# Kernel tuning notes

Measured on AMD Instinct MI355X. Metric: run time of the kernel, lower is better.

The kernel has to match this reference:

```python
import jax, jax.numpy as jnp
import numpy as np

B, C, H, W = 4, 64, 64, 64

def setup_inputs() -> dict:
    key = jax.random.key(0)
    ks = jax.random.split(key, 7)
    s = 1.0 / np.sqrt(C)
    return {
        "x": jax.random.normal(ks[0], (B, C, H, W), dtype=jnp.float32),
        "Wq": jax.random.normal(ks[1], (C, C), dtype=jnp.float32) * s,
        "bq": jax.random.normal(ks[2], (C,), dtype=jnp.float32) * s,
        "Wk": jax.random.normal(ks[3], (C, C), dtype=jnp.float32) * s,
        "bk": jax.random.normal(ks[4], (C,), dtype=jnp.float32) * s,
        "Wv": jax.random.normal(ks[5], (C, C), dtype=jnp.float32) * s,
        "bv": jax.random.normal(ks[6], (C,), dtype=jnp.float32) * s,
    }

def reference(x, Wq, bq, Wk, bk, Wv, bv):
    b, c, h, w = x.shape
    n = h * w
    xf = x.reshape(b, c, n)                                   # (B,C,N)
    # 1x1 convs == per-pixel linear maps over channels
    q = jnp.einsum('oc,bcn->bon', Wq, xf) + bq[None, :, None]  # (B,C,N)
    k = jnp.einsum('oc,bcn->bon', Wk, xf) + bk[None, :, None]  # (B,C,N)
    v = jnp.einsum('oc,bcn->bon', Wv, xf) + bv[None, :, None]  # (B,C,N)
    # energy = Q^T K : (B,N,N); note: no 1/sqrt(C) scaling in the original
    energy = jnp.einsum('bcn,bcm->bnm', q, k)
    attention = jax.nn.softmax(energy, axis=-1)
    # out = V @ attention^T : out[:, :, i] = sum_j V[:, :, j] * attention[i, j]
    out = jnp.einsum('bcm,bnm->bcn', v, attention)
    return out.reshape(b, c, h, w)
```

## Files before the change

kernel.cpp:

```cpp
#include <hip/hip_runtime.h>
#include <math.h>

#define T_N 4096
#define T_C 64
#define T_B 4
#define NSLICE 4
#define TILES_PER_SLICE (64 / NSLICE)

typedef __attribute__((ext_vector_type(8))) _Float16 f16x8;
typedef __attribute__((ext_vector_type(4))) _Float16 f16x4;
typedef __attribute__((ext_vector_type(4))) float f32x4;

__device__ inline unsigned short f2h(float f) {
    union { _Float16 h; unsigned short s; } u; u.h = (_Float16)f; return u.s;
}
__device__ inline float h2f(unsigned short s) {
    union { unsigned short s; _Float16 h; } u; u.s = s; return (float)u.h;
}

__global__ __launch_bounds__(256) void qkv_kernel(
    const float* __restrict__ x,
    const float* __restrict__ Wq, const float* __restrict__ bq,
    const float* __restrict__ Wk, const float* __restrict__ bk,
    const float* __restrict__ Wv, const float* __restrict__ bv,
    unsigned short* __restrict__ qt_hi, unsigned short* __restrict__ qt_lo,
    unsigned short* __restrict__ kt, unsigned short* __restrict__ vb)
{
    __shared__ __align__(16) unsigned short xsh[64 * 72];
    __shared__ __align__(16) unsigned short xsl[64 * 72];
    __shared__ __align__(16) unsigned short wf[64 * 72];

    const int tid = threadIdx.x;
    const int n0  = blockIdx.x * 64;
    const int b   = blockIdx.y;
    const int p   = blockIdx.z;
    const float* W    = (p == 0) ? Wq : (p == 1) ? Wk : Wv;
    const float* bias = (p == 0) ? bq : (p == 1) ? bk : bv;
    const float* xb   = x + (size_t)b * T_C * T_N;

    for (int i = tid; i < 1024; i += 256) {
        const int o = i >> 4, c4 = (i & 15) * 4;
        const float4 w4 = ((const float4*)W)[i];
        f16x4 wh;
        wh[0] = (_Float16)w4.x; wh[1] = (_Float16)w4.y;
        wh[2] = (_Float16)w4.z; wh[3] = (_Float16)w4.w;
        *(f16x4*)&wf[o * 72 + c4] = wh;
    }
    for (int i = tid; i < 1024; i += 256) {
        const int c = i >> 4, nj4 = (i & 15) * 4;
        const float4 xv = *(const float4*)&xb[c * T_N + n0 + nj4];
        const float xa[4] = {xv.x, xv.y, xv.z, xv.w};
        #pragma unroll
        for (int j = 0; j < 4; ++j) {
            const unsigned short h = f2h(xa[j]);
            xsh[(nj4 + j) * 72 + c] = h;
            xsl[(nj4 + j) * 72 + c] = f2h(xa[j] - h2f(h));
        }
    }
    __syncthreads();

    const int wv_  = tid >> 6;
    const int lane = tid & 63;
    const int quad = lane >> 4;
    const int col  = lane & 15;
    const size_t bN = (size_t)b * T_N;

    f16x8 xh[2], xl[2];
    #pragma unroll
    for (int s = 0; s < 2; ++s) {
        xh[s] = *(const f16x8*)&xsh[(wv_ * 16 + col) * 72 + s * 32 + quad * 8];
        xl[s] = *(const f16x8*)&xsl[(wv_ * 16 + col) * 72 + s * 32 + quad * 8];
    }

    #pragma unroll
    for (int osub = 0; osub < 4; ++osub) {
        f32x4 acc = (f32x4){0.f, 0.f, 0.f, 0.f};
        #pragma unroll
        for (int s = 0; s < 2; ++s) {
            const f16x8 wfr = *(const f16x8*)&wf[(osub * 16 + col) * 72 + s * 32 + quad * 8];
            acc = __builtin_amdgcn_mfma_f32_16x16x32_f16(xh[s], wfr, acc, 0, 0, 0);
            acc = __builtin_amdgcn_mfma_f32_16x16x32_f16(xl[s], wfr, acc, 0, 0, 0);
        }
        const float bb = bias[osub * 16 + col];
        if (p == 0) {
            #pragma unroll
            for (int r = 0; r < 4; ++r) {
                const float f = acc[r] + bb;
                const unsigned short h = f2h(f);
                const size_t off = (bN + n0 + wv_ * 16 + quad * 4 + r) * 64 + osub * 16 + col;
                qt_hi[off] = h;
                qt_lo[off] = f2h(f - h2f(h));
            }
        } else if (p == 1) {
            #pragma unroll
            for (int r = 0; r < 4; ++r)
                kt[(bN + n0 + wv_ * 16 + quad * 4 + r) * 64 + osub * 16 + col] =
                    f2h(acc[r] + bb);
        } else {
            union { ushort4 v; unsigned short s[4]; } hv;
            #pragma unroll
            for (int r = 0; r < 4; ++r) hv.s[r] = f2h(acc[r] + bb);
            *(ushort4*)&vb[((size_t)(b * 64 + osub * 16 + col)) * T_N +
                           n0 + wv_ * 16 + quad * 4] = hv.v;
        }
    }
}

__global__ __launch_bounds__(256, 4) void attn_kernel(
    const unsigned short* __restrict__ qt_hi, const unsigned short* __restrict__ qt_lo,
    const unsigned short* __restrict__ kt, const unsigned short* __restrict__ vb,
    unsigned short* __restrict__ o_part, float* __restrict__ mp, float* __restrict__ lp)
{
    __shared__ __align__(16) unsigned short ks[64 * 72];
    __shared__ __align__(16) unsigned short vs[64 * 72];

    const int tid   = threadIdx.x;
    const int n0    = blockIdx.x * 64;
    const int slice = blockIdx.y;
    const int b     = blockIdx.z;
    const int wv_   = tid >> 6;
    const int lane  = tid & 63;
    const int quad  = lane >> 4;
    const int col   = lane & 15;

    const size_t bN = (size_t)b * T_N;
    const int q_own = n0 + wv_ * 16 + col;

    f16x8 qh[2], ql[2];
    #pragma unroll
    for (int s = 0; s < 2; ++s) {
        const size_t qoff = (bN + q_own) * 64 + s * 32 + quad * 8;
        qh[s] = *(const f16x8*)&qt_hi[qoff];
        ql[s] = *(const f16x8*)&qt_lo[qoff];
    }

    f32x4 O[4];
    #pragma unroll
    for (int t = 0; t < 4; ++t) O[t] = (f32x4){0.f, 0.f, 0.f, 0.f};
    float m_st = -INFINITY, l_st = 0.f;

    for (int it = 0; it < TILES_PER_SLICE; ++it) {
        const int m0 = (slice * TILES_PER_SLICE + it) * 64;
        __syncthreads();
        for (int i = tid; i < 1024; i += 256) {
            if (i < 512) {
                const int row = i >> 3, cc = i & 7;
                *(float4*)&ks[row * 72 + cc * 8] =
                    *(const float4*)&kt[(bN + m0 + row) * 64 + cc * 8];
            } else {
                const int j = i - 512, row = j >> 3, cc = j & 7;
                *(float4*)&vs[row * 72 + cc * 8] =
                    *(const float4*)&vb[((size_t)(b * 64 + row)) * T_N + m0 + cc * 8];
            }
        }
        __syncthreads();

        f32x4 acc[4];
        #pragma unroll
        for (int t = 0; t < 4; ++t) acc[t] = (f32x4){0.f, 0.f, 0.f, 0.f};
        #pragma unroll
        for (int s = 0; s < 2; ++s) {
            #pragma unroll
            for (int t = 0; t < 4; ++t) {
                const f16x8 kf =
                    *(const f16x8*)&ks[(t * 16 + col) * 72 + s * 32 + quad * 8];
                acc[t] = __builtin_amdgcn_mfma_f32_16x16x32_f16(kf, qh[s], acc[t], 0, 0, 0);
                acc[t] = __builtin_amdgcn_mfma_f32_16x16x32_f16(kf, ql[s], acc[t], 0, 0, 0);
            }
        }

        float mx = -INFINITY;
        #pragma unroll
        for (int t = 0; t < 4; ++t)
            #pragma unroll
            for (int r = 0; r < 4; ++r) mx = fmaxf(mx, acc[t][r]);
        mx = fmaxf(mx, __shfl_xor(mx, 16));
        mx = fmaxf(mx, __shfl_xor(mx, 32));
        const float mnew = fmaxf(m_st, mx);
        const float alpha = __expf(m_st - mnew);
        float sum = 0.f;
        f16x4 pf[4];
        #pragma unroll
        for (int t = 0; t < 4; ++t) {
            #pragma unroll
            for (int r = 0; r < 4; ++r) {
                const float pv = __expf(acc[t][r] - mnew);
                sum += pv;
                pf[t][r] = (_Float16)pv;
            }
        }
        sum += __shfl_xor(sum, 16);
        sum += __shfl_xor(sum, 32);
        l_st = alpha * l_st + sum;
        m_st = mnew;

        #pragma unroll
        for (int tc = 0; tc < 4; ++tc) {
            O[tc] *= alpha;
            #pragma unroll
            for (int t = 0; t < 4; ++t) {
                const f16x4 vf =
                    *(const f16x4*)&vs[(tc * 16 + col) * 72 + t * 16 + quad * 4];
                O[tc] = __builtin_amdgcn_mfma_f32_16x16x16f16(vf, pf[t], O[tc], 0, 0, 0);
            }
        }
    }

    #pragma unroll
    for (int tc = 0; tc < 4; ++tc) {
        #pragma unroll
        for (int r = 0; r < 4; ++r) {
            o_part[((size_t)((slice * T_B + b) * 64 + tc * 16 + quad * 4 + r)) * T_N +
                   q_own] = f2h(O[tc][r]);
        }
    }
    if (quad == 0) {
        const size_t off = (size_t)(slice * T_B + b) * T_N + q_own;
        mp[off] = m_st;
        lp[off] = l_st;
    }
}

__global__ __launch_bounds__(256) void combine_kernel(
    const unsigned short* __restrict__ o_part,
    const float* __restrict__ mp, const float* __restrict__ lp,
    float* __restrict__ out)
{
    __shared__ float wn[NSLICE][32];

    const int tid = threadIdx.x;
    const int n0  = blockIdx.x * 32;
    const int b   = blockIdx.y;

    if (tid < 32) {
        float m_s[NSLICE], l_s[NSLICE];
        #pragma unroll
        for (int s = 0; s < NSLICE; ++s) {
            const size_t off = (size_t)(s * T_B + b) * T_N + n0 + tid;
            m_s[s] = mp[off];
            l_s[s] = lp[off];
        }
        float M = m_s[0];
        #pragma unroll
        for (int s = 1; s < NSLICE; ++s) M = fmaxf(M, m_s[s]);
        float w_s[NSLICE], L = 0.f;
        #pragma unroll
        for (int s = 0; s < NSLICE; ++s) {
            w_s[s] = __expf(m_s[s] - M);
            L += l_s[s] * w_s[s];
        }
        const float inv = 1.f / L;
        #pragma unroll
        for (int s = 0; s < NSLICE; ++s) wn[s][tid] = w_s[s] * inv;
    }
    __syncthreads();

    for (int t = tid; t < 512; t += 256) {
        const int c = t >> 3, g = t & 7;
        float4 acc = make_float4(0.f, 0.f, 0.f, 0.f);
        #pragma unroll
        for (int s = 0; s < NSLICE; ++s) {
            const ushort4 o4 = *(const ushort4*)
                &o_part[((size_t)((s * T_B + b) * 64 + c)) * T_N + n0 + g * 4];
            acc.x = fmaf(h2f(o4.x), wn[s][g * 4 + 0], acc.x);
            acc.y = fmaf(h2f(o4.y), wn[s][g * 4 + 1], acc.y);
            acc.z = fmaf(h2f(o4.z), wn[s][g * 4 + 2], acc.z);
            acc.w = fmaf(h2f(o4.w), wn[s][g * 4 + 3], acc.w);
        }
        *(float4*)&out[((size_t)(b * 64 + c)) * T_N + n0 + g * 4] = acc;
    }
}

extern "C" void kernel_launch(void* const* d_in, const int* in_sizes, int n_in,
                              void* d_out, int out_size, void* d_ws, size_t ws_size,
                              hipStream_t stream) {
    const float* x  = (const float*)d_in[0];
    const float* Wq = (const float*)d_in[1];
    const float* bq = (const float*)d_in[2];
    const float* Wk = (const float*)d_in[3];
    const float* bk = (const float*)d_in[4];
    const float* Wv = (const float*)d_in[5];
    const float* bv = (const float*)d_in[6];
    float* outp = (float*)d_out;

    const size_t elems = (size_t)T_B * T_N * T_C;
    unsigned short* qt_hi  = (unsigned short*)d_ws;
    unsigned short* qt_lo  = qt_hi + elems;
    unsigned short* ktp    = qt_lo + elems;
    unsigned short* vbuf   = ktp + elems;
    unsigned short* o_part = vbuf + elems;
    float* mp = (float*)(o_part + (size_t)NSLICE * elems);
    float* lp = mp + (size_t)NSLICE * T_B * T_N;

    qkv_kernel<<<dim3(T_N / 64, T_B, 3), 256, 0, stream>>>(
        x, Wq, bq, Wk, bk, Wv, bv, qt_hi, qt_lo, ktp, vbuf);
    attn_kernel<<<dim3(T_N / 64, NSLICE, T_B), 256, 0, stream>>>(
        qt_hi, qt_lo, ktp, vbuf, o_part, mp, lp);
    combine_kernel<<<dim3(T_N / 32, T_B), 256, 0, stream>>>(
        o_part, mp, lp, outp);
}
```

Before: 130.2 us.

## Fuse Q/K/V projections per block and stage outputs through LDS for coalesced stores

```diff
diff --git a/kernel.cpp b/kernel.cpp
--- a/kernel.cpp
+++ b/kernel.cpp
@@ -26,28 +26,29 @@
     unsigned short* __restrict__ qt_hi, unsigned short* __restrict__ qt_lo,
     unsigned short* __restrict__ kt, unsigned short* __restrict__ vb)
 {
-    __shared__ __align__(16) unsigned short xsh[64 * 72];
-    __shared__ __align__(16) unsigned short xsl[64 * 72];
-    __shared__ __align__(16) unsigned short wf[64 * 72];
+    __shared__ __align__(16) unsigned short xsh[32 * 72];
+    __shared__ __align__(16) unsigned short xsl[32 * 72];
+    __shared__ __align__(16) unsigned short wf[3][64 * 72];
 
     const int tid = threadIdx.x;
-    const int n0  = blockIdx.x * 64;
+    const int n0  = blockIdx.x * 32;
     const int b   = blockIdx.y;
-    const int p   = blockIdx.z;
-    const float* W    = (p == 0) ? Wq : (p == 1) ? Wk : Wv;
-    const float* bias = (p == 0) ? bq : (p == 1) ? bk : bv;
-    const float* xb   = x + (size_t)b * T_C * T_N;
-
-    for (int i = tid; i < 1024; i += 256) {
-        const int o = i >> 4, c4 = (i & 15) * 4;
-        const float4 w4 = ((const float4*)W)[i];
-        f16x4 wh;
-        wh[0] = (_Float16)w4.x; wh[1] = (_Float16)w4.y;
-        wh[2] = (_Float16)w4.z; wh[3] = (_Float16)w4.w;
-        *(f16x4*)&wf[o * 72 + c4] = wh;
-    }
-    for (int i = tid; i < 1024; i += 256) {
-        const int c = i >> 4, nj4 = (i & 15) * 4;
+    const float* xb = x + (size_t)b * T_C * T_N;
+
+    const float* Ws[3] = {Wq, Wk, Wv};
+    #pragma unroll
+    for (int p = 0; p < 3; ++p) {
+        for (int i = tid; i < 1024; i += 256) {
+            const int o = i >> 4, c4 = (i & 15) * 4;
+            const float4 w4 = ((const float4*)Ws[p])[i];
+            f16x4 wh;
+            wh[0] = (_Float16)w4.x; wh[1] = (_Float16)w4.y;
+            wh[2] = (_Float16)w4.z; wh[3] = (_Float16)w4.w;
+            *(f16x4*)&wf[p][o * 72 + c4] = wh;
+        }
+    }
+    for (int i = tid; i < 512; i += 256) {
+        const int c = i >> 3, nj4 = (i & 7) * 4;
         const float4 xv = *(const float4*)&xb[c * T_N + n0 + nj4];
         const float xa[4] = {xv.x, xv.y, xv.z, xv.w};
         #pragma unroll
@@ -63,46 +64,66 @@
     const int lane = tid & 63;
     const int quad = lane >> 4;
     const int col  = lane & 15;
+    const int pst  = (wv_ & 1) * 16;
+    const int oh   = (wv_ >> 1) * 2;
     const size_t bN = (size_t)b * T_N;
 
     f16x8 xh[2], xl[2];
     #pragma unroll
     for (int s = 0; s < 2; ++s) {
-        xh[s] = *(const f16x8*)&xsh[(wv_ * 16 + col) * 72 + s * 32 + quad * 8];
-        xl[s] = *(const f16x8*)&xsl[(wv_ * 16 + col) * 72 + s * 32 + quad * 8];
-    }
-
-    #pragma unroll
-    for (int osub = 0; osub < 4; ++osub) {
-        f32x4 acc = (f32x4){0.f, 0.f, 0.f, 0.f};
-        #pragma unroll
-        for (int s = 0; s < 2; ++s) {
-            const f16x8 wfr = *(const f16x8*)&wf[(osub * 16 + col) * 72 + s * 32 + quad * 8];
-            acc = __builtin_amdgcn_mfma_f32_16x16x32_f16(xh[s], wfr, acc, 0, 0, 0);
-            acc = __builtin_amdgcn_mfma_f32_16x16x32_f16(xl[s], wfr, acc, 0, 0, 0);
-        }
-        const float bb = bias[osub * 16 + col];
+        xh[s] = *(const f16x8*)&xsh[(pst + col) * 72 + s * 32 + quad * 8];
+        xl[s] = *(const f16x8*)&xsl[(pst + col) * 72 + s * 32 + quad * 8];
+    }
+    __syncthreads();
+
+    const float* biases[3] = {bq, bk, bv};
+    for (int p = 0; p < 3; ++p) {
+        #pragma unroll
+        for (int oo = 0; oo < 2; ++oo) {
+            const int osub = oh + oo;
+            f32x4 acc = (f32x4){0.f, 0.f, 0.f, 0.f};
+            #pragma unroll
+            for (int s = 0; s < 2; ++s) {
+                const f16x8 wfr =
+                    *(const f16x8*)&wf[p][(osub * 16 + col) * 72 + s * 32 + quad * 8];
+                acc = __builtin_amdgcn_mfma_f32_16x16x32_f16(xh[s], wfr, acc, 0, 0, 0);
+                acc = __builtin_amdgcn_mfma_f32_16x16x32_f16(xl[s], wfr, acc, 0, 0, 0);
+            }
+            const float bb = biases[p][osub * 16 + col];
+            if (p == 0) {
+                #pragma unroll
+                for (int r = 0; r < 4; ++r) {
+                    const float f = acc[r] + bb;
+                    const unsigned short h = f2h(f);
+                    const int a = (pst + quad * 4 + r) * 72 + osub * 16 + col;
+                    xsh[a] = h;
+                    xsl[a] = f2h(f - h2f(h));
+                }
+            } else if (p == 1) {
+                #pragma unroll
+                for (int r = 0; r < 4; ++r)
+                    xsh[(pst + quad * 4 + r) * 72 + osub * 16 + col] = f2h(acc[r] + bb);
+            } else {
+                union { ushort4 v; unsigned short s[4]; } hv;
+                #pragma unroll
+                for (int r = 0; r < 4; ++r) hv.s[r] = f2h(acc[r] + bb);
+                *(ushort4*)&xsh[(osub * 16 + col) * 36 + pst + quad * 4] = hv.v;
+            }
+        }
+        __syncthreads();
         if (p == 0) {
-            #pragma unroll
-            for (int r = 0; r < 4; ++r) {
-                const float f = acc[r] + bb;
-                const unsigned short h = f2h(f);
-                const size_t off = (bN + n0 + wv_ * 16 + quad * 4 + r) * 64 + osub * 16 + col;
-                qt_hi[off] = h;
-                qt_lo[off] = f2h(f - h2f(h));
-            }
+            const int pix = tid >> 3, c8 = (tid & 7) * 8;
+            *(f16x8*)&qt_hi[(bN + n0 + pix) * 64 + c8] = *(const f16x8*)&xsh[pix * 72 + c8];
+            *(f16x8*)&qt_lo[(bN + n0 + pix) * 64 + c8] = *(const f16x8*)&xsl[pix * 72 + c8];
         } else if (p == 1) {
-            #pragma unroll
-            for (int r = 0; r < 4; ++r)
-                kt[(bN + n0 + wv_ * 16 + quad * 4 + r) * 64 + osub * 16 + col] =
-                    f2h(acc[r] + bb);
+            const int pix = tid >> 3, c8 = (tid & 7) * 8;
+            *(f16x8*)&kt[(bN + n0 + pix) * 64 + c8] = *(const f16x8*)&xsh[pix * 72 + c8];
         } else {
-            union { ushort4 v; unsigned short s[4]; } hv;
-            #pragma unroll
-            for (int r = 0; r < 4; ++r) hv.s[r] = f2h(acc[r] + bb);
-            *(ushort4*)&vb[((size_t)(b * 64 + osub * 16 + col)) * T_N +
-                           n0 + wv_ * 16 + quad * 4] = hv.v;
-        }
+            const int o = tid >> 2, p8 = (tid & 3) * 8;
+            *(f16x8*)&vb[((size_t)(b * 64 + o)) * T_N + n0 + p8] =
+                *(const f16x8*)&xsh[o * 36 + p8];
+        }
+        if (p < 2) __syncthreads();
     }
 }
 
@@ -292,7 +313,7 @@
     float* mp = (float*)(o_part + (size_t)NSLICE * elems);
     float* lp = mp + (size_t)NSLICE * T_B * T_N;
 
-    qkv_kernel<<<dim3(T_N / 64, T_B, 3), 256, 0, stream>>>(
+    qkv_kernel<<<dim3(T_N / 32, T_B), 256, 0, stream>>>(
         x, Wq, bq, Wk, bk, Wv, bv, qt_hi, qt_lo, ktp, vbuf);
     attn_kernel<<<dim3(T_N / 64, NSLICE, T_B), 256, 0, stream>>>(
         qt_hi, qt_lo, ktp, vbuf, o_part, mp, lp);
```

Measured after the change: 129.7 us. No clear change (-0.4%).
